# Kernel tuning notes

Hardware: AMD Instinct MI355X
Metric: run time of the kernel (lower is better)

## Reference

```python
import jax, jax.numpy as jnp
import numpy as np
import math

TAU_PLUS = 20.0
TAU_MINUS = 20.0
A_PLUS = 0.01
A_MINUS = 0.01
W_MAX = 1.0
W_MIN = 0.0
TARGET_RATE = 0.1
HOMEO = 0.001
RATE_ALPHA = 0.01
DT = 1.0


def setup_inputs() -> dict:
    key = jax.random.key(0)
    k1, k2, k3, k4 = jax.random.split(key, 4)
    B, PRE, POST = 1024, 4096, 4096
    return {
        "pre_spikes": jax.random.uniform(k1, (B, PRE), dtype=jnp.float32),
        "post_spikes": jax.random.uniform(k2, (B, POST), dtype=jnp.float32),
        "weights": jax.random.uniform(k3, (POST, PRE), dtype=jnp.float32) * 0.5,
        "pre_trace": jnp.zeros((B, PRE), dtype=jnp.float32),
        "post_trace": jnp.zeros((B, POST), dtype=jnp.float32),
        "running_rate": jax.random.uniform(k4, (POST,), dtype=jnp.float32) * 0.2,
    }


def reference(pre_spikes, post_spikes, weights, pre_trace, post_trace, running_rate):
    B = pre_spikes.shape[0]
    # trace decay
    pre_tr = pre_trace * math.exp(-DT / TAU_PLUS)
    post_tr = post_trace * math.exp(-DT / TAU_MINUS)
    # STDP weight update (learn=True, auto_scale=False)
    dw_plus = A_PLUS * jnp.einsum('bp,bq->pq', post_spikes, pre_tr) / B
    dw_minus = -A_MINUS * jnp.einsum('bp,bq->pq', post_tr, pre_spikes) / B
    dw_homeo = -HOMEO * (running_rate - TARGET_RATE)[:, None]
    new_weights = jnp.clip(weights + dw_plus + dw_minus + dw_homeo, W_MIN, W_MAX)
    # homeostatic rate EMA
    batch_rate = post_spikes.mean(axis=0)
    new_rate = running_rate * (1.0 - RATE_ALPHA) + RATE_ALPHA * batch_rate
    # trace update
    new_pre_trace = pre_tr + pre_spikes
    new_post_trace = post_tr + post_spikes
    # postsynaptic current with updated weights
    current = pre_spikes @ new_weights.T  # (B, POST)
    return current, new_weights, new_pre_trace, new_post_trace, new_rate
```

## Files before the change

kernel.cpp:

```cpp
#include <hip/hip_runtime.h>
#include <hip/hip_fp8.h>

typedef __attribute__((ext_vector_type(8))) short short8;
typedef __attribute__((ext_vector_type(4))) float floatx4;
typedef __attribute__((ext_vector_type(8))) int int8v;
typedef __attribute__((ext_vector_type(4))) int int4v;

#define LDS_PTR(x) ((__attribute__((address_space(3))) unsigned int*)(x))
#define GLB_PTR(x) ((const __attribute__((address_space(1))) unsigned int*)(x))

__device__ __forceinline__ unsigned short f2bf(float f) {
    unsigned int u = __float_as_uint(f);
    unsigned int r = (u + 0x7FFFu + ((u >> 16) & 1u)) >> 16;
    return (unsigned short)r;
}
__device__ __forceinline__ unsigned char f2fp8(float f) {
    __hip_fp8_e4m3 v(f);
    return (unsigned char)v.__x;
}
__device__ __forceinline__ float fp82f(unsigned int u) {
    __hip_fp8_e4m3 v;
    v.__x = (__hip_fp8_storage_t)(u & 0xFF);
    return (float)v;
}

__global__ __launch_bounds__(256) void prep_post_kernel(
    const float* __restrict__ S, const float* __restrict__ T,
    float* __restrict__ traceOut, unsigned char* __restrict__ At,
    int C, int K2, int Bsz, float dp)
{
    __shared__ float sT[64][65];
    __shared__ float tT[64][65];
    const int t = threadIdx.x;
    const int r0 = blockIdx.y * 64, c0 = blockIdx.x * 64;
#pragma unroll
    for (int i = 0; i < 4; ++i) {
        int rl = (t >> 4) + i * 16;
        int cl = (t & 15) * 4;
        size_t g = (size_t)(r0 + rl) * C + c0 + cl;
        float4 s4 = *(const float4*)&S[g];
        float4 t4 = *(const float4*)&T[g];
        float4 o;
        o.x = fmaf(t4.x, dp, s4.x); o.y = fmaf(t4.y, dp, s4.y);
        o.z = fmaf(t4.z, dp, s4.z); o.w = fmaf(t4.w, dp, s4.w);
        *(float4*)&traceOut[g] = o;
        sT[rl][cl + 0] = s4.x; sT[rl][cl + 1] = s4.y;
        sT[rl][cl + 2] = s4.z; sT[rl][cl + 3] = s4.w;
        tT[rl][cl + 0] = t4.x; tT[rl][cl + 1] = t4.y;
        tT[rl][cl + 2] = t4.z; tT[rl][cl + 3] = t4.w;
    }
    __syncthreads();
#pragma unroll
    for (int i = 0; i < 4; ++i) {
        int cl = (t >> 4) + i * 16;
        int rl = (t & 15) * 4;
        uchar4 a, b;
        a.x = f2fp8(sT[rl + 0][cl]); a.y = f2fp8(sT[rl + 1][cl]);
        a.z = f2fp8(sT[rl + 2][cl]); a.w = f2fp8(sT[rl + 3][cl]);
        b.x = f2fp8(tT[rl + 0][cl]); b.y = f2fp8(tT[rl + 1][cl]);
        b.z = f2fp8(tT[rl + 2][cl]); b.w = f2fp8(tT[rl + 3][cl]);
        *(uchar4*)&At[(size_t)(c0 + cl) * K2 + r0 + rl] = a;
        *(uchar4*)&At[(size_t)(c0 + cl) * K2 + Bsz + r0 + rl] = b;
    }
}

__global__ __launch_bounds__(256) void prep_pre_kernel(
    const float* __restrict__ S, const float* __restrict__ T,
    float* __restrict__ traceOut, unsigned char* __restrict__ Bt,
    unsigned short* __restrict__ preBf,
    int C, int K2, int Bsz, float dp)
{
    __shared__ float sT[64][65];
    __shared__ float tT[64][65];
    const int t = threadIdx.x;
    const int r0 = blockIdx.y * 64, c0 = blockIdx.x * 64;
#pragma unroll
    for (int i = 0; i < 4; ++i) {
        int rl = (t >> 4) + i * 16;
        int cl = (t & 15) * 4;
        size_t g = (size_t)(r0 + rl) * C + c0 + cl;
        float4 s4 = *(const float4*)&S[g];
        float4 t4 = *(const float4*)&T[g];
        float4 o;
        o.x = fmaf(t4.x, dp, s4.x); o.y = fmaf(t4.y, dp, s4.y);
        o.z = fmaf(t4.z, dp, s4.z); o.w = fmaf(t4.w, dp, s4.w);
        *(float4*)&traceOut[g] = o;
        ushort4 pb = { f2bf(s4.x), f2bf(s4.y), f2bf(s4.z), f2bf(s4.w) };
        *(ushort4*)&preBf[g] = pb;
        sT[rl][cl + 0] = s4.x; sT[rl][cl + 1] = s4.y;
        sT[rl][cl + 2] = s4.z; sT[rl][cl + 3] = s4.w;
        tT[rl][cl + 0] = t4.x; tT[rl][cl + 1] = t4.y;
        tT[rl][cl + 2] = t4.z; tT[rl][cl + 3] = t4.w;
    }
    __syncthreads();
#pragma unroll
    for (int i = 0; i < 4; ++i) {
        int cl = (t >> 4) + i * 16;
        int rl = (t & 15) * 4;
        uchar4 a, b;
        a.x = f2fp8(tT[rl + 0][cl]); a.y = f2fp8(tT[rl + 1][cl]);
        a.z = f2fp8(tT[rl + 2][cl]); a.w = f2fp8(tT[rl + 3][cl]);
        b.x = f2fp8(-sT[rl + 0][cl]); b.y = f2fp8(-sT[rl + 1][cl]);
        b.z = f2fp8(-sT[rl + 2][cl]); b.w = f2fp8(-sT[rl + 3][cl]);
        *(uchar4*)&Bt[(size_t)(c0 + cl) * K2 + r0 + rl] = a;
        *(uchar4*)&Bt[(size_t)(c0 + cl) * K2 + Bsz + r0 + rl] = b;
    }
}

__global__ __launch_bounds__(256) void rate_kernel(
    const unsigned char* __restrict__ At, const float* __restrict__ rr,
    float* __restrict__ new_rate, int K2, int Bsz)
{
    const int w = threadIdx.x >> 6, l = threadIdx.x & 63;
    const int p = blockIdx.x * 4 + w;
    const unsigned char* row = At + (size_t)p * K2;
    float s = 0.f;
    for (int k = l * 16; k < Bsz; k += 1024) {
        int4v v = *(const int4v*)&row[k];
#pragma unroll
        for (int wd = 0; wd < 4; ++wd) {
            unsigned int u = (unsigned int)v[wd];
            s += fp82f(u) + fp82f(u >> 8) + fp82f(u >> 16) + fp82f(u >> 24);
        }
    }
#pragma unroll
    for (int off = 32; off > 0; off >>= 1) s += __shfl_xor(s, off, 64);
    if (l == 0)
        new_rate[p] = rr[p] * 0.99f + 0.01f * (s / (float)Bsz);
}

__global__ __launch_bounds__(256) void dw_fp8_kernel(
    const unsigned char* __restrict__ A, const unsigned char* __restrict__ B,
    int K, int N, float s,
    const float* __restrict__ Wold, const float* __restrict__ rr,
    float* __restrict__ outF, unsigned short* __restrict__ outBf)
{
    constexpr int BM = 128, BN = 128, BK = 128;
    __shared__ unsigned char smem[65536];

    const int t = threadIdx.x;
    const int l = t & 63;
    const int w = t >> 6;
    const int wm = w >> 1, wn = w & 1;
    const int bm = blockIdx.y, bn = blockIdx.x;

    floatx4 acc[4][4] = {};

    auto stage = [&](int buf, int k0) {
        unsigned char* la = smem + buf * 16384;
        unsigned char* lb = smem + 32768 + buf * 16384;
#pragma unroll
        for (int i = 0; i < 4; ++i) {
            int ci = i * 256 + t;
            int r = ci >> 3, sc = ci & 7;
            int g = sc ^ (r & 7);
            const unsigned char* gpA = A + (size_t)(bm * BM + r) * K + k0 + g * 16;
            __builtin_amdgcn_global_load_lds(GLB_PTR(gpA),
                LDS_PTR(la + ci * 16), 16, 0, 0);
            const unsigned char* gpB = B + (size_t)(bn * BN + r) * K + k0 + g * 16;
            __builtin_amdgcn_global_load_lds(GLB_PTR(gpB),
                LDS_PTR(lb + ci * 16), 16, 0, 0);
        }
    };

    stage(0, 0);
    __syncthreads();

    const int nT = K / BK;
    int cur = 0;
    for (int tt = 0; tt < nT; ++tt) {
        if (tt + 1 < nT) stage(cur ^ 1, (tt + 1) * BK);

        const unsigned char* la = smem + cur * 16384;
        const unsigned char* lb = smem + 32768 + cur * 16384;
        const int c = l >> 4;
        const int m = l & 15;
        int8v af[4], bf[4];
#pragma unroll
        for (int i = 0; i < 4; ++i) {
            int ra = wm * 64 + i * 16 + m;
            int s0 = (2 * c) ^ (ra & 7), s1 = (2 * c + 1) ^ (ra & 7);
            int4v lo = *(const int4v*)&la[ra * BK + s0 * 16];
            int4v hi = *(const int4v*)&la[ra * BK + s1 * 16];
            af[i][0] = lo[0]; af[i][1] = lo[1]; af[i][2] = lo[2]; af[i][3] = lo[3];
            af[i][4] = hi[0]; af[i][5] = hi[1]; af[i][6] = hi[2]; af[i][7] = hi[3];
        }
#pragma unroll
        for (int j = 0; j < 4; ++j) {
            int rb = wn * 64 + j * 16 + m;
            int s0 = (2 * c) ^ (rb & 7), s1 = (2 * c + 1) ^ (rb & 7);
            int4v lo = *(const int4v*)&lb[rb * BK + s0 * 16];
            int4v hi = *(const int4v*)&lb[rb * BK + s1 * 16];
            bf[j][0] = lo[0]; bf[j][1] = lo[1]; bf[j][2] = lo[2]; bf[j][3] = lo[3];
            bf[j][4] = hi[0]; bf[j][5] = hi[1]; bf[j][6] = hi[2]; bf[j][7] = hi[3];
        }
#pragma unroll
        for (int i = 0; i < 4; ++i)
#pragma unroll
            for (int j = 0; j < 4; ++j)
                acc[i][j] = __builtin_amdgcn_mfma_scale_f32_16x16x128_f8f6f4(
                    af[i], bf[j], acc[i][j], 0, 0, 0, 0x7f, 0, 0x7f);

        asm volatile("s_waitcnt vmcnt(0)" ::: "memory");
        __builtin_amdgcn_s_barrier();
        cur ^= 1;
    }

    __syncthreads();
    float* sOut = (float*)smem;
#pragma unroll
    for (int i = 0; i < 4; ++i)
#pragma unroll
        for (int r = 0; r < 4; ++r) {
            const int row = wm * 64 + i * 16 + (l >> 4) * 4 + r;
#pragma unroll
            for (int j = 0; j < 4; ++j) {
                const int col = wn * 64 + j * 16 + (l & 15);
                sOut[row * 128 + col] = acc[i][j][r];
            }
        }
    __syncthreads();

    const int pBase = bm * BM;
    const int qBase = bn * BN;
#pragma unroll
    for (int k = 0; k < 16; ++k) {
        const int ci = k * 256 + t;
        const int row = ci >> 5;
        const int cc = (ci & 31) * 4;
        const int p = pBase + row;
        const int q = qBase + cc;
        const size_t idx = (size_t)p * N + q;
        float4 a4 = *(const float4*)&sOut[ci * 4];
        float4 w4 = *(const float4*)&Wold[idx];
        const float hp = -0.001f * (rr[p] - 0.1f);
        float4 v;
        v.x = fminf(fmaxf(fmaf(s, a4.x, w4.x + hp), 0.f), 1.f);
        v.y = fminf(fmaxf(fmaf(s, a4.y, w4.y + hp), 0.f), 1.f);
        v.z = fminf(fmaxf(fmaf(s, a4.z, w4.z + hp), 0.f), 1.f);
        v.w = fminf(fmaxf(fmaf(s, a4.w, w4.w + hp), 0.f), 1.f);
        *(float4*)&outF[idx] = v;
        ushort4 b4 = { f2bf(v.x), f2bf(v.y), f2bf(v.z), f2bf(v.w) };
        *(ushort4*)&outBf[idx] = b4;
    }
}

__global__ __launch_bounds__(512) void mfma_gemm_bt(
    const unsigned short* __restrict__ A,
    const unsigned short* __restrict__ Bm,
    int K, int N, float* __restrict__ outF)
{
    constexpr int BM = 128, BN = 128, BK = 128;
    __shared__ unsigned char smem[131072];

    const int t = threadIdx.x;
    const int l = t & 63;
    const int w = t >> 6;
    const int wm = w >> 2, wn = w & 3;
    const int bm = blockIdx.y, bn = blockIdx.x;

    floatx4 acc[4][2] = {};

    auto stage = [&](int buf, int k0) {
        unsigned short* la = (unsigned short*)(smem + buf * 65536);
        unsigned short* lb = (unsigned short*)(smem + buf * 65536 + 32768);
#pragma unroll
        for (int i = 0; i < 4; ++i) {
            int ci = i * 512 + t;
            int r = ci >> 4, sc = ci & 15;
            int g = sc ^ (r & 15);
            const unsigned short* gpA =
                A + (size_t)(bm * BM + r) * K + k0 + g * 8;
            __builtin_amdgcn_global_load_lds(GLB_PTR(gpA),
                LDS_PTR(la + ci * 8), 16, 0, 0);
            const unsigned short* gpB =
                Bm + (size_t)(bn * BN + r) * K + k0 + g * 8;
            __builtin_amdgcn_global_load_lds(GLB_PTR(gpB),
                LDS_PTR(lb + ci * 8), 16, 0, 0);
        }
    };

    stage(0, 0);
    __syncthreads();

    const int nT = K / BK;
    int cur = 0;
    for (int tt = 0; tt < nT; ++tt) {
        if (tt + 1 < nT) stage(cur ^ 1, (tt + 1) * BK);

        const unsigned short* la = (const unsigned short*)(smem + cur * 65536);
        const unsigned short* lb = (const unsigned short*)(smem + cur * 65536 + 32768);
        const int q = l >> 4;
        const int m = l & 15;
#pragma unroll
        for (int ks = 0; ks < 4; ++ks) {
            short8 af[4], bf[2];
            const int c2 = ks * 4 + q;
#pragma unroll
            for (int i = 0; i < 4; ++i) {
                int ra = wm * 64 + i * 16 + m;
                af[i] = *(const short8*)&la[ra * BK + ((c2 ^ (ra & 15)) * 8)];
            }
#pragma unroll
            for (int j = 0; j < 2; ++j) {
                int rb = wn * 32 + j * 16 + m;
                bf[j] = *(const short8*)&lb[rb * BK + ((c2 ^ (rb & 15)) * 8)];
            }
#pragma unroll
            for (int i = 0; i < 4; ++i)
#pragma unroll
                for (int j = 0; j < 2; ++j)
                    acc[i][j] = __builtin_amdgcn_mfma_f32_16x16x32_bf16(
                        af[i], bf[j], acc[i][j], 0, 0, 0);
        }

        asm volatile("s_waitcnt vmcnt(0)" ::: "memory");
        __builtin_amdgcn_s_barrier();
        cur ^= 1;
    }

    __syncthreads();
    float* sOut = (float*)smem;
#pragma unroll
    for (int i = 0; i < 4; ++i)
#pragma unroll
        for (int r = 0; r < 4; ++r) {
            const int row = wm * 64 + i * 16 + (l >> 4) * 4 + r;
#pragma unroll
            for (int j = 0; j < 2; ++j) {
                const int col = wn * 32 + j * 16 + (l & 15);
                sOut[row * 128 + col] = acc[i][j][r];
            }
        }
    __syncthreads();

    const int pBase = bm * BM;
    const int qBase = bn * BN;
#pragma unroll
    for (int k = 0; k < 8; ++k) {
        const int ci = k * 512 + t;
        const int row = ci >> 5;
        const int cc = (ci & 31) * 4;
        float4 v = *(const float4*)&sOut[ci * 4];
        *(float4*)&outF[(size_t)(pBase + row) * N + qBase + cc] = v;
    }
}

extern "C" void kernel_launch(void* const* d_in, const int* in_sizes, int n_in,
                              void* d_out, int out_size, void* d_ws, size_t ws_size,
                              hipStream_t stream)
{
    const float* pre_spikes   = (const float*)d_in[0];
    const float* post_spikes  = (const float*)d_in[1];
    const float* weights      = (const float*)d_in[2];
    const float* pre_trace    = (const float*)d_in[3];
    const float* post_trace   = (const float*)d_in[4];
    const float* running_rate = (const float*)d_in[5];

    const int POST = in_sizes[5];
    const int PRE  = in_sizes[2] / POST;
    const int Bsz  = in_sizes[0] / PRE;
    const int K2   = 2 * Bsz;

    const size_t nCur   = (size_t)Bsz * POST;
    const size_t nW     = (size_t)POST * PRE;
    const size_t nPreT  = (size_t)Bsz * PRE;
    const size_t nPostT = (size_t)Bsz * POST;

    float* out_current    = (float*)d_out;
    float* out_weights    = out_current + nCur;
    float* out_pre_trace  = out_weights + nW;
    float* out_post_trace = out_pre_trace + nPreT;
    float* out_rate       = out_post_trace + nPostT;

    unsigned char* At     = (unsigned char*)d_ws;
    unsigned char* Bt     = At + (size_t)POST * K2;
    unsigned short* preBf = (unsigned short*)(Bt + (size_t)PRE * K2);
    unsigned short* wBf   = preBf + nPreT;

    const float dp = 0.95122942450071400910f;
    const float s  = dp * (0.01f / (float)Bsz);

    prep_post_kernel<<<dim3(POST / 64, Bsz / 64), 256, 0, stream>>>(
        post_spikes, post_trace, out_post_trace, At, POST, K2, Bsz, dp);
    prep_pre_kernel<<<dim3(PRE / 64, Bsz / 64), 256, 0, stream>>>(
        pre_spikes, pre_trace, out_pre_trace, Bt, preBf, PRE, K2, Bsz, dp);

    rate_kernel<<<POST / 4, 256, 0, stream>>>(
        At, running_rate, out_rate, K2, Bsz);

    dw_fp8_kernel<<<dim3(PRE / 128, POST / 128), 256, 0, stream>>>(
        At, Bt, K2, PRE, s, weights, running_rate, out_weights, wBf);

    mfma_gemm_bt<<<dim3(POST / 128, Bsz / 128), 512, 0, stream>>>(
        preBf, wBf, PRE, POST, out_current);
}
```

Before: 297.3 us.

## Enlarge dw tile to 256x128 with triple-buffered interleaved LDS staging

```diff
diff --git a/kernel.cpp b/kernel.cpp
--- a/kernel.cpp
+++ b/kernel.cpp
@@ -129,14 +129,14 @@
         new_rate[p] = rr[p] * 0.99f + 0.01f * (s / (float)Bsz);
 }
 
-__global__ __launch_bounds__(256) void dw_fp8_kernel(
+__global__ __launch_bounds__(512) void dw_fp8_kernel(
     const unsigned char* __restrict__ A, const unsigned char* __restrict__ B,
     int K, int N, float s,
     const float* __restrict__ Wold, const float* __restrict__ rr,
     float* __restrict__ outF, unsigned short* __restrict__ outBf)
 {
-    constexpr int BM = 128, BN = 128, BK = 128;
-    __shared__ unsigned char smem[65536];
+    constexpr int BM = 256, BN = 128, BK = 128;
+    __shared__ unsigned char smem[147456];
 
     const int t = threadIdx.x;
     const int l = t & 63;
@@ -146,64 +146,99 @@
 
     floatx4 acc[4][4] = {};
 
-    auto stage = [&](int buf, int k0) {
-        unsigned char* la = smem + buf * 16384;
-        unsigned char* lb = smem + 32768 + buf * 16384;
-#pragma unroll
-        for (int i = 0; i < 4; ++i) {
-            int ci = i * 256 + t;
+    auto stageA = [&](int buf, int k0, int half) {
+        unsigned char* la = smem + buf * 49152;
+#pragma unroll
+        for (int i = 0; i < 2; ++i) {
+            int ci = half * 1024 + i * 512 + t;
             int r = ci >> 3, sc = ci & 7;
             int g = sc ^ (r & 7);
-            const unsigned char* gpA = A + (size_t)(bm * BM + r) * K + k0 + g * 16;
-            __builtin_amdgcn_global_load_lds(GLB_PTR(gpA),
+            const unsigned char* gp = A + (size_t)(bm * BM + r) * K + k0 + g * 16;
+            __builtin_amdgcn_global_load_lds(GLB_PTR(gp),
                 LDS_PTR(la + ci * 16), 16, 0, 0);
-            const unsigned char* gpB = B + (size_t)(bn * BN + r) * K + k0 + g * 16;
-            __builtin_amdgcn_global_load_lds(GLB_PTR(gpB),
+        }
+    };
+    auto stageB = [&](int buf, int k0) {
+        unsigned char* lb = smem + buf * 49152 + 32768;
+#pragma unroll
+        for (int i = 0; i < 2; ++i) {
+            int ci = i * 512 + t;
+            int r = ci >> 3, sc = ci & 7;
+            int g = sc ^ (r & 7);
+            const unsigned char* gp = B + (size_t)(bn * BN + r) * K + k0 + g * 16;
+            __builtin_amdgcn_global_load_lds(GLB_PTR(gp),
                 LDS_PTR(lb + ci * 16), 16, 0, 0);
         }
     };
 
-    stage(0, 0);
-    __syncthreads();
+    const int kq = l >> 4;
+    const int m = l & 15;
+
+    auto rdfrag = [&](const unsigned char* base, int row) {
+        int s0 = (2 * kq) ^ (row & 7), s1 = (2 * kq + 1) ^ (row & 7);
+        int4v lo = *(const int4v*)&base[row * 128 + s0 * 16];
+        int4v hi = *(const int4v*)&base[row * 128 + s1 * 16];
+        int8v r;
+        r[0] = lo[0]; r[1] = lo[1]; r[2] = lo[2]; r[3] = lo[3];
+        r[4] = hi[0]; r[5] = hi[1]; r[6] = hi[2]; r[7] = hi[3];
+        return r;
+    };
 
     const int nT = K / BK;
-    int cur = 0;
+    stageA(0, 0, 0); stageA(0, 0, 1); stageB(0, 0);
+    stageA(1, BK, 0); stageA(1, BK, 1); stageB(1, BK);
+    asm volatile("s_waitcnt vmcnt(6)" ::: "memory");
+    __builtin_amdgcn_s_barrier();
+
+    int c = 0;
     for (int tt = 0; tt < nT; ++tt) {
-        if (tt + 1 < nT) stage(cur ^ 1, (tt + 1) * BK);
-
-        const unsigned char* la = smem + cur * 16384;
-        const unsigned char* lb = smem + 32768 + cur * 16384;
-        const int c = l >> 4;
-        const int m = l & 15;
-        int8v af[4], bf[4];
-#pragma unroll
-        for (int i = 0; i < 4; ++i) {
-            int ra = wm * 64 + i * 16 + m;
-            int s0 = (2 * c) ^ (ra & 7), s1 = (2 * c + 1) ^ (ra & 7);
-            int4v lo = *(const int4v*)&la[ra * BK + s0 * 16];
-            int4v hi = *(const int4v*)&la[ra * BK + s1 * 16];
-            af[i][0] = lo[0]; af[i][1] = lo[1]; af[i][2] = lo[2]; af[i][3] = lo[3];
-            af[i][4] = hi[0]; af[i][5] = hi[1]; af[i][6] = hi[2]; af[i][7] = hi[3];
-        }
-#pragma unroll
-        for (int j = 0; j < 4; ++j) {
-            int rb = wn * 64 + j * 16 + m;
-            int s0 = (2 * c) ^ (rb & 7), s1 = (2 * c + 1) ^ (rb & 7);
-            int4v lo = *(const int4v*)&lb[rb * BK + s0 * 16];
-            int4v hi = *(const int4v*)&lb[rb * BK + s1 * 16];
-            bf[j][0] = lo[0]; bf[j][1] = lo[1]; bf[j][2] = lo[2]; bf[j][3] = lo[3];
-            bf[j][4] = hi[0]; bf[j][5] = hi[1]; bf[j][6] = hi[2]; bf[j][7] = hi[3];
-        }
+        const unsigned char* la = smem + c * 49152;
+        const unsigned char* lb = smem + c * 49152 + 32768;
+        int n2 = c + 2; if (n2 >= 3) n2 -= 3;
+        const int k2 = (tt + 2) * BK;
+        const bool doStage = (tt + 2 < nT);
+
+        int8v af[4], bfj;
+
 #pragma unroll
         for (int i = 0; i < 4; ++i)
-#pragma unroll
-            for (int j = 0; j < 4; ++j)
+            af[i] = rdfrag(la, wm * 64 + i * 16 + m);
+        bfj = rdfrag(lb, wn * 64 + m);
+        __builtin_amdgcn_s_barrier();
+        asm volatile("s_waitcnt lgkmcnt(0)" ::: "memory");
+        __builtin_amdgcn_sched_barrier(0);
+        __builtin_amdgcn_s_setprio(1);
+#pragma unroll
+        for (int i = 0; i < 4; ++i)
+            acc[i][0] = __builtin_amdgcn_mfma_scale_f32_16x16x128_f8f6f4(
+                af[i], bfj, acc[i][0], 0, 0, 0, 0x7f, 0, 0x7f);
+        __builtin_amdgcn_s_setprio(0);
+        __builtin_amdgcn_s_barrier();
+
+#pragma unroll
+        for (int j = 1; j < 4; ++j) {
+            if (doStage) {
+                if (j == 1)      stageA(n2, k2, 0);
+                else if (j == 2) stageA(n2, k2, 1);
+                else             stageB(n2, k2);
+            }
+            bfj = rdfrag(lb, wn * 64 + j * 16 + m);
+            __builtin_amdgcn_s_barrier();
+            asm volatile("s_waitcnt lgkmcnt(0)" ::: "memory");
+            __builtin_amdgcn_sched_barrier(0);
+            __builtin_amdgcn_s_setprio(1);
+#pragma unroll
+            for (int i = 0; i < 4; ++i)
                 acc[i][j] = __builtin_amdgcn_mfma_scale_f32_16x16x128_f8f6f4(
-                    af[i], bf[j], acc[i][j], 0, 0, 0, 0x7f, 0, 0x7f);
-
-        asm volatile("s_waitcnt vmcnt(0)" ::: "memory");
+                    af[i], bfj, acc[i][j], 0, 0, 0, 0x7f, 0, 0x7f);
+            __builtin_amdgcn_s_setprio(0);
+            if (j < 3) __builtin_amdgcn_s_barrier();
+        }
+
+        if (doStage) asm volatile("s_waitcnt vmcnt(6)" ::: "memory");
+        else         asm volatile("s_waitcnt vmcnt(0)" ::: "memory");
         __builtin_amdgcn_s_barrier();
-        cur ^= 1;
+        c = (c + 1 == 3) ? 0 : c + 1;
     }
 
     __syncthreads();
@@ -225,7 +260,7 @@
     const int qBase = bn * BN;
 #pragma unroll
     for (int k = 0; k < 16; ++k) {
-        const int ci = k * 256 + t;
+        const int ci = k * 512 + t;
         const int row = ci >> 5;
         const int cc = (ci & 31) * 4;
         const int p = pBase + row;
@@ -389,7 +424,7 @@
     rate_kernel<<<POST / 4, 256, 0, stream>>>(
         At, running_rate, out_rate, K2, Bsz);
 
-    dw_fp8_kernel<<<dim3(PRE / 128, POST / 128), 256, 0, stream>>>(
+    dw_fp8_kernel<<<dim3(PRE / 128, POST / 256), 512, 0, stream>>>(
         At, Bt, K2, PRE, s, weights, running_rate, out_weights, wBf);
 
     mfma_gemm_bt<<<dim3(POST / 128, Bsz / 128), 512, 0, stream>>>(
```

Result: slower. 309.7 us (+4.2%).
